# Optimization experiments

Measured on AMD Instinct MI355X. Metric: run time of the kernel, lower is better.

The kernel has to match this reference:

```python
import jax, jax.numpy as jnp
import numpy as np

B, S, IN_DIM, OUT_DIM, G = 8, 2048, 512, 256, 8
CHUNK = 128  # positions per scan step; per-chunk phi = CHUNK*O*O*G floats
EPS = 1e-5   # torch LayerNorm default


def make_periods():
    # periods[i,j,g] = i*(O*G) + j*G + g + 2
    i = jnp.arange(OUT_DIM, dtype=jnp.float32)[:, None, None]
    j = jnp.arange(OUT_DIM, dtype=jnp.float32)[None, :, None]
    g = jnp.arange(G, dtype=jnp.float32)[None, None, :]
    return i * (OUT_DIM * G) + j * G + g + 2.0


def setup_inputs() -> dict:
    key = jax.random.key(0)
    ks = jax.random.split(key, 4)
    x = jax.random.normal(ks[0], (B, S, IN_DIM), dtype=jnp.float32)
    positions = jnp.arange(S, dtype=jnp.int64 if jax.config.jax_enable_x64 else jnp.int32)
    M = jax.random.uniform(ks[1], (OUT_DIM, IN_DIM), minval=-0.5, maxval=0.5, dtype=jnp.float32)
    P = jax.random.uniform(ks[2], (OUT_DIM, OUT_DIM, G), minval=-0.1, maxval=0.1, dtype=jnp.float32)
    W_res = jax.random.uniform(ks[3], (OUT_DIM, IN_DIM), minval=-0.1, maxval=0.1, dtype=jnp.float32)
    ln_scale = jnp.ones((OUT_DIM,), dtype=jnp.float32)
    ln_bias = jnp.zeros((OUT_DIM,), dtype=jnp.float32)
    periods = make_periods()
    return {"x": x, "M": M, "P": P, "W_res": W_res, "ln_scale": ln_scale,
            "ln_bias": ln_bias, "periods": periods, "positions": positions}


def layer_norm(h, scale, bias):
    mu = jnp.mean(h, axis=-1, keepdims=True)
    var = jnp.mean(jnp.square(h - mu), axis=-1, keepdims=True)  # biased, like torch
    return (h - mu) * jax.lax.rsqrt(var + EPS) * scale + bias


def reference(x, M, P, W_res, ln_scale, ln_bias, periods, positions):
    # x: (B,S,in), M: (out,in), P: (out,out,G), periods: (out,out,G)
    x_trans = layer_norm(jnp.einsum('bsi,oi->bso', x, M), ln_scale, ln_bias)

    two_pi = jnp.float32(2.0 * np.pi)
    pos_chunks = positions.astype(jnp.float32).reshape(-1, CHUNK)  # (S/CHUNK, CHUNK)

    def body(carry, pos):
        # phi: (CHUNK, O, O, G); reduce over g first to avoid the huge 5D tensor
        phi = jnp.cos(two_pi * pos[:, None, None, None] / periods)
        A = jnp.einsum('sijg,ijg->sij', phi, P)  # (CHUNK, O, O)
        return carry, A

    _, A = jax.lax.scan(body, 0, pos_chunks)
    A = A.reshape(S, OUT_DIM, OUT_DIM)  # A[s,i,j] = sum_g P[i,j,g]*cos(2*pi*k_s/T_ijg)

    Nk = jnp.einsum('bsj,sij->bsi', x_trans, A)  # (B,S,out)
    residual = jnp.einsum('bsi,oi->bso', x, W_res)  # separate residual proj
    return Nk + residual
```

## Files before the change

### kernel.cpp

```cpp
#include <hip/hip_runtime.h>
#include <hip/hip_bf16.h>
#include <math.h>

#define B_   8
#define S_   2048
#define IN_  512
#define OUT_ 256
#define G_   8


typedef float  f32x4  __attribute__((ext_vector_type(4)));
typedef short  s16x8  __attribute__((ext_vector_type(8)));
typedef __bf16 bf16x8 __attribute__((ext_vector_type(8)));
typedef unsigned short u16x8 __attribute__((ext_vector_type(8)));

__device__ __forceinline__ float cos2pi(float f) {
#if __has_builtin(__builtin_amdgcn_cosf)
    return __builtin_amdgcn_cosf(f);
#else
    return __cosf(6.28318530717958647692f * f);
#endif
}

__device__ __forceinline__ float fractf_(float f) {
#if __has_builtin(__builtin_amdgcn_fractf)
    return __builtin_amdgcn_fractf(f);
#else
    return f - floorf(f);
#endif
}

__device__ __forceinline__ unsigned short f2bf(float f) {
    unsigned u = __builtin_bit_cast(unsigned, f);
    u += 0x7fffu + ((u >> 16) & 1u);
    return (unsigned short)(u >> 16);
}

template <typename T>
__device__ __forceinline__ auto mfma_bf16_(T a, T b, f32x4 c, int)
    -> decltype(__builtin_amdgcn_mfma_f32_16x16x32_bf16(a, b, c, 0, 0, 0)) {
    return __builtin_amdgcn_mfma_f32_16x16x32_bf16(a, b, c, 0, 0, 0);
}
template <typename T>
__device__ __forceinline__ auto mfma_bf16_(T a, T b, f32x4 c, long)
    -> decltype(__builtin_amdgcn_mfma_f32_16x16x32_bf16(__builtin_bit_cast(bf16x8, a),
                                                        __builtin_bit_cast(bf16x8, b), c, 0, 0, 0)) {
    return __builtin_amdgcn_mfma_f32_16x16x32_bf16(__builtin_bit_cast(bf16x8, a),
                                                   __builtin_bit_cast(bf16x8, b), c, 0, 0, 0);
}
__device__ __forceinline__ f32x4 mfma_bf16(s16x8 a, s16x8 b, f32x4 c) {
    return mfma_bf16_(a, b, c, 0);
}

__device__ __forceinline__ void gld16(const void* g, void* l) {
    __builtin_amdgcn_global_load_lds((const __attribute__((address_space(1))) unsigned int*)g,
                                     (__attribute__((address_space(3))) unsigned int*)l,
                                     16, 0, 0);
}

__global__ __launch_bounds__(256) void cvt_x(const float* __restrict__ x,
                                             unsigned short* __restrict__ Xb) {
    const int idx = blockIdx.x * 256 + threadIdx.x;
    const float4 v0 = *(const float4*)(x + (size_t)idx * 8);
    const float4 v1 = *(const float4*)(x + (size_t)idx * 8 + 4);
    u16x8 o;
    o[0] = f2bf(v0.x); o[1] = f2bf(v0.y); o[2] = f2bf(v0.z); o[3] = f2bf(v0.w);
    o[4] = f2bf(v1.x); o[5] = f2bf(v1.y); o[6] = f2bf(v1.z); o[7] = f2bf(v1.w);
    *(u16x8*)(Xb + (size_t)idx * 8) = o;
}

__global__ __launch_bounds__(256) void cvt_w(const float* __restrict__ M,
                                             const float* __restrict__ Wres,
                                             unsigned short* __restrict__ Wb) {
    const int idx = blockIdx.x * 256 + threadIdx.x;
    const int row = idx >> 6;
    const int col = (idx & 63) * 8;
    const float* src = (row < 256) ? (M + (size_t)row * 512 + col)
                                   : (Wres + (size_t)(row - 256) * 512 + col);
    const float4 v0 = *(const float4*)(src);
    const float4 v1 = *(const float4*)(src + 4);
    u16x8 o;
    o[0] = f2bf(v0.x); o[1] = f2bf(v0.y); o[2] = f2bf(v0.z); o[3] = f2bf(v0.w);
    o[4] = f2bf(v1.x); o[5] = f2bf(v1.y); o[6] = f2bf(v1.z); o[7] = f2bf(v1.w);
    *(u16x8*)(Wb + (size_t)row * 512 + col) = o;
}

__global__ __launch_bounds__(256) void gemm_mfma(const unsigned short* __restrict__ Xb,
                                                 const unsigned short* __restrict__ Wb,
                                                 float* __restrict__ y,
                                                 float* __restrict__ out) {
    __shared__ __align__(16) unsigned short At[128 * 64];
    __shared__ __align__(16) unsigned short Bt[128 * 64];
    const int t    = threadIdx.x;
    const int col0 = blockIdx.x * 128;
    const int row0 = blockIdx.y * 128;

    const unsigned short* ga[4];
    const unsigned short* gb[4];
    int lofs[4];
#pragma unroll
    for (int cc = 0; cc < 4; ++cc) {
        const int L = cc * 256 + t;
        const int r = L >> 3;
        const int c = (L & 7) ^ (r & 7);
        ga[cc]   = Xb + (size_t)(row0 + r) * 512 + c * 8;
        gb[cc]   = Wb + (size_t)(col0 + r) * 512 + c * 8;
        lofs[cc] = L * 8;
    }

    const int lane = t & 63;
    const int wave = t >> 6;
    const int wm   = (wave & 1) * 64;
    const int wn   = (wave >> 1) * 64;
    const int quad = lane >> 4;
    const int l16  = lane & 15;

    f32x4 acc[4][4];
#pragma unroll
    for (int mi = 0; mi < 4; ++mi)
#pragma unroll
        for (int ni = 0; ni < 4; ++ni) acc[mi][ni] = {0.0f, 0.0f, 0.0f, 0.0f};

    for (int k0 = 0; k0 < 512; k0 += 64) {
        __syncthreads();
#pragma unroll
        for (int cc = 0; cc < 4; ++cc) {
            gld16(ga[cc] + k0, At + lofs[cc]);
            gld16(gb[cc] + k0, Bt + lofs[cc]);
        }
        __syncthreads();
#pragma unroll
        for (int ks = 0; ks < 2; ++ks) {
            s16x8 af[4], bf[4];
#pragma unroll
            for (int mi = 0; mi < 4; ++mi) {
                const int cc = (ks * 4 + quad) ^ (l16 & 7);
                const int ra = wm + mi * 16 + l16;
                const int rb = wn + mi * 16 + l16;
                af[mi] = *(const s16x8*)(At + (ra * 8 + cc) * 8);
                bf[mi] = *(const s16x8*)(Bt + (rb * 8 + cc) * 8);
            }
#pragma unroll
            for (int mi = 0; mi < 4; ++mi)
#pragma unroll
                for (int ni = 0; ni < 4; ++ni)
                    acc[mi][ni] = mfma_bf16(af[mi], bf[ni], acc[mi][ni]);
        }
    }

    float* dst   = (col0 < 256) ? y : out;
    const int cb = (col0 & 255) + wn;
#pragma unroll
    for (int mi = 0; mi < 4; ++mi) {
        const int rbase = row0 + wm + mi * 16 + quad * 4;
#pragma unroll
        for (int ni = 0; ni < 4; ++ni) {
            const int col = cb + ni * 16 + l16;
#pragma unroll
            for (int rg = 0; rg < 4; ++rg)
                dst[(size_t)(rbase + rg) * 256 + col] = acc[mi][ni][rg];
        }
    }
}

__global__ __launch_bounds__(256) void gemm_kernel(const float* __restrict__ x,
                                                   const float* __restrict__ M,
                                                   const float* __restrict__ Wres,
                                                   float* __restrict__ y,
                                                   float* __restrict__ out) {
    __shared__ float As[8][132];
    __shared__ float Bs[8][132];
    const int ct = blockIdx.x;
    const int rt = blockIdx.y;
    const int t  = threadIdx.x;
    const int row0 = rt * 128;
    const float* W = (ct < 2) ? M : Wres;
    const int wcol0 = (ct & 1) * 128;
    float acc[8][8];
#pragma unroll
    for (int r = 0; r < 8; ++r)
#pragma unroll
        for (int c = 0; c < 8; ++c) acc[r][c] = 0.0f;
    const int lr = t >> 1;
    const int lk = (t & 1) << 2;
    for (int k0 = 0; k0 < 512; k0 += 8) {
        float4 av = *(const float4*)(x + (size_t)(row0 + lr) * 512 + k0 + lk);
        float4 bv = *(const float4*)(W + (size_t)(wcol0 + lr) * 512 + k0 + lk);
        __syncthreads();
        As[lk + 0][lr] = av.x; As[lk + 1][lr] = av.y; As[lk + 2][lr] = av.z; As[lk + 3][lr] = av.w;
        Bs[lk + 0][lr] = bv.x; Bs[lk + 1][lr] = bv.y; Bs[lk + 2][lr] = bv.z; Bs[lk + 3][lr] = bv.w;
        __syncthreads();
        const int tx = t & 15, ty = t >> 4;
#pragma unroll
        for (int kk = 0; kk < 8; ++kk) {
            const float4 a0 = *(const float4*)&As[kk][ty * 8];
            const float4 a1 = *(const float4*)&As[kk][ty * 8 + 4];
            const float4 b0 = *(const float4*)&Bs[kk][tx * 8];
            const float4 b1 = *(const float4*)&Bs[kk][tx * 8 + 4];
            const float ar[8] = {a0.x, a0.y, a0.z, a0.w, a1.x, a1.y, a1.z, a1.w};
            const float br[8] = {b0.x, b0.y, b0.z, b0.w, b1.x, b1.y, b1.z, b1.w};
#pragma unroll
            for (int r = 0; r < 8; ++r)
#pragma unroll
                for (int c = 0; c < 8; ++c) acc[r][c] = fmaf(ar[r], br[c], acc[r][c]);
        }
    }
    const int tx = t & 15, ty = t >> 4;
    float* dst = (ct < 2) ? y : out;
    const int cbase = (ct & 1) * 128 + tx * 8;
#pragma unroll
    for (int r = 0; r < 8; ++r) {
        float4 v0 = {acc[r][0], acc[r][1], acc[r][2], acc[r][3]};
        float4 v1 = {acc[r][4], acc[r][5], acc[r][6], acc[r][7]};
        float* p = dst + (size_t)(row0 + ty * 8 + r) * 256 + cbase;
        *(float4*)(p)     = v0;
        *(float4*)(p + 4) = v1;
    }
}

__global__ __launch_bounds__(256) void ln_kernel(float* __restrict__ y,
                                                 const float* __restrict__ scale,
                                                 const float* __restrict__ bias) {
    const int t    = threadIdx.x;
    const int row  = blockIdx.x * 4 + (t >> 6);
    const int lane = t & 63;
    float* p = y + (size_t)row * 256 + lane * 4;
    float4 v = *(float4*)p;
    float s  = v.x + v.y + v.z + v.w;
    float ss = v.x * v.x + v.y * v.y + v.z * v.z + v.w * v.w;
#pragma unroll
    for (int off = 32; off > 0; off >>= 1) {
        s  += __shfl_xor(s, off);
        ss += __shfl_xor(ss, off);
    }
    const float mu  = s * (1.0f / 256.0f);
    const float var = ss * (1.0f / 256.0f) - mu * mu;
    const float rs  = rsqrtf(var + 1e-5f);
    float4 sc = *(const float4*)(scale + lane * 4);
    float4 bi = *(const float4*)(bias + lane * 4);
    float4 o;
    o.x = (v.x - mu) * rs * sc.x + bi.x;
    o.y = (v.y - mu) * rs * sc.y + bi.y;
    o.z = (v.z - mu) * rs * sc.z + bi.z;
    o.w = (v.w - mu) * rs * sc.w + bi.w;
    *(float4*)p = o;
}

__global__ __launch_bounds__(256) void prep_ptk(const float* __restrict__ P,
                                                const float* __restrict__ periods,
                                                float4* __restrict__ PTK) {
    const int tid = blockIdx.x * 256 + threadIdx.x;
    const int j = tid >> 8, i = tid & 255;
    float p[8], iT[8], k2[8];
#pragma unroll
    for (int g = 0; g < 8; ++g) {
        const int idx = (i * 256 + j) * 8 + g;
        p[g]  = P[idx];
        iT[g] = 1.0f / periods[idx];
        k2[g] = 2.0f * cos2pi(iT[g]);
    }
    float4* base = PTK + (size_t)(j * 6) * 256 + i;
    base[0]    = make_float4(p[0], iT[0], p[1], iT[1]);
    base[256]  = make_float4(p[2], iT[2], p[3], iT[3]);
    base[512]  = make_float4(p[4], iT[4], p[5], iT[5]);
    base[768]  = make_float4(p[6], iT[6], p[7], iT[7]);
    base[1024] = make_float4(k2[0], k2[1], k2[2], k2[3]);
    base[1280] = make_float4(k2[4], k2[5], k2[6], k2[7]);
}

__global__ __launch_bounds__(256, 2) void cosnk8(const float4* __restrict__ PTK,
                                                 const float* __restrict__ xt,
                                                 float* __restrict__ out) {
    __shared__ float xs[256][64];
    const int t  = threadIdx.x;
    const int bx = blockIdx.x;
    const int ih = (bx >> 2) & 1;
    const int stile = ((bx >> 3) << 2) | (bx & 3);
    const int s0 = stile * 8;

    {
        const int slot = t >> 2;
        const int st   = slot >> 3;
        const int b    = slot & 7;
        const int jb   = (t & 3) * 64;
        const float* src = xt + (size_t)(b * S_ + s0 + st) * 256 + jb;
#pragma unroll
        for (int q = 0; q < 16; ++q) {
            float4 v = *(const float4*)(src + 4 * q);
            xs[jb + 4 * q + 0][slot] = v.x;
            xs[jb + 4 * q + 1][slot] = v.y;
            xs[jb + 4 * q + 2][slot] = v.z;
            xs[jb + 4 * q + 3][slot] = v.w;
        }
    }
    __syncthreads();

    const int i  = ih * 128 + (t & 127);
    const int jh = t >> 7;
    const int j0 = jh * 128;
    const float sv0 = (float)s0;

    float acc[8][8];
#pragma unroll
    for (int s = 0; s < 8; ++s)
#pragma unroll
        for (int b = 0; b < 8; ++b) acc[s][b] = 0.0f;

    const float4* ptk = PTK + (size_t)(j0 * 6) * 256 + i;
    float4 q0 = ptk[0],    q1 = ptk[256],  q2 = ptk[512];
    float4 q3 = ptk[768], k01 = ptk[1024], k23 = ptk[1280];

#define CHEB8(p_, iT_, k2_)                         \
    do {                                            \
        float f0 = fractf_(sv0 * (iT_));            \
        float c0 = cos2pi(f0);                      \
        float c1 = cos2pi(fractf_(f0 + (iT_)));     \
        float c2 = fmaf((k2_), c1, -c0);            \
        float c3 = fmaf((k2_), c2, -c1);            \
        float c4 = fmaf((k2_), c3, -c2);            \
        float c5 = fmaf((k2_), c4, -c3);            \
        float c6 = fmaf((k2_), c5, -c4);            \
        float c7 = fmaf((k2_), c6, -c5);            \
        a0 = fmaf((p_), c0, a0); a1 = fmaf((p_), c1, a1); \
        a2 = fmaf((p_), c2, a2); a3 = fmaf((p_), c3, a3); \
        a4 = fmaf((p_), c4, a4); a5 = fmaf((p_), c5, a5); \
        a6 = fmaf((p_), c6, a6); a7 = fmaf((p_), c7, a7); \
    } while (0)

    for (int jj = 0; jj < 128; ++jj) {
        const float4* pn = ptk + ((jj < 127) ? 1536 : 0);
        const float4 n0 = pn[0],   n1 = pn[256],  n2 = pn[512];
        const float4 n3 = pn[768], n4 = pn[1024], n5 = pn[1280];

        float a0 = 0.f, a1 = 0.f, a2 = 0.f, a3 = 0.f, a4 = 0.f, a5 = 0.f, a6 = 0.f, a7 = 0.f;
        CHEB8(q0.x, q0.y, k01.x);
        CHEB8(q0.z, q0.w, k01.y);
        CHEB8(q1.x, q1.y, k01.z);
        CHEB8(q1.z, q1.w, k01.w);
        CHEB8(q2.x, q2.y, k23.x);
        CHEB8(q2.z, q2.w, k23.y);
        CHEB8(q3.x, q3.y, k23.z);
        CHEB8(q3.z, q3.w, k23.w);

        const float* xrow = &xs[j0 + jj][0];
        const float as_[8] = {a0, a1, a2, a3, a4, a5, a6, a7};
#pragma unroll
        for (int s = 0; s < 8; ++s) {
            const float4 xa = *(const float4*)(xrow + s * 8);
            const float4 xb = *(const float4*)(xrow + s * 8 + 4);
            acc[s][0] = fmaf(as_[s], xa.x, acc[s][0]);
            acc[s][1] = fmaf(as_[s], xa.y, acc[s][1]);
            acc[s][2] = fmaf(as_[s], xa.z, acc[s][2]);
            acc[s][3] = fmaf(as_[s], xa.w, acc[s][3]);
            acc[s][4] = fmaf(as_[s], xb.x, acc[s][4]);
            acc[s][5] = fmaf(as_[s], xb.y, acc[s][5]);
            acc[s][6] = fmaf(as_[s], xb.z, acc[s][6]);
            acc[s][7] = fmaf(as_[s], xb.w, acc[s][7]);
        }
        q0 = n0; q1 = n1; q2 = n2; q3 = n3; k01 = n4; k23 = n5;
        ptk = pn;
    }
#undef CHEB8

    __syncthreads();
    float* red = &xs[0][0];
    const int tl = t & 127;
    if (jh) {
#pragma unroll
        for (int slot = 0; slot < 64; ++slot)
            red[slot * 128 + tl] = acc[slot >> 3][slot & 7];
    }
    __syncthreads();
    if (!jh) {
#pragma unroll
        for (int slot = 0; slot < 64; ++slot) {
            const int st = slot >> 3, b = slot & 7;
            const float v = acc[st][b] + red[slot * 128 + tl];
            out[(size_t)(b * S_ + s0 + st) * 256 + i] += v;
        }
    }
}

extern "C" void kernel_launch(void* const* d_in, const int* in_sizes, int n_in,
                              void* d_out, int out_size, void* d_ws, size_t ws_size,
                              hipStream_t stream) {
    const float* x        = (const float*)d_in[0];
    const float* M        = (const float*)d_in[1];
    const float* P        = (const float*)d_in[2];
    const float* Wres     = (const float*)d_in[3];
    const float* ln_scale = (const float*)d_in[4];
    const float* ln_bias  = (const float*)d_in[5];
    const float* periods  = (const float*)d_in[6];

    float* out = (float*)d_out;
    char*  wsb = (char*)d_ws;
    float* y   = (float*)wsb;
    unsigned short* Xb = (unsigned short*)(wsb + (size_t)16 * 1024 * 1024);
    float4* PTK        = (float4*)(wsb + (size_t)16 * 1024 * 1024);
    unsigned short* Wb = (unsigned short*)(wsb + (size_t)32 * 1024 * 1024);

    const bool use_mfma = (ws_size >= (size_t)34078720);

    if (use_mfma) {
        cvt_x<<<4096, 256, 0, stream>>>(x, Xb);
        cvt_w<<<128, 256, 0, stream>>>(M, Wres, Wb);
        dim3 ggrid(4, 128);
        gemm_mfma<<<ggrid, 256, 0, stream>>>(Xb, Wb, y, out);
    } else {
        dim3 ggrid(4, 128);
        gemm_kernel<<<ggrid, 256, 0, stream>>>(x, M, Wres, y, out);
    }

    ln_kernel<<<4096, 256, 0, stream>>>(y, ln_scale, ln_bias);

    prep_ptk<<<256, 256, 0, stream>>>(P, periods, PTK);

    cosnk8<<<512, 256, 0, stream>>>(PTK, y, out);
}
```

Baseline: 235.5 us.

## Split cosine kernel over j halves with atomics, shrink GEMM tile, merge conversions

The cosine/Nk kernel now splits the j reduction across two blocks, giving 1024 blocks with smaller shared memory and a higher occupancy target. Partial sums go into the output with float atomics instead of a plain read-modify-write. The MFMA GEMM moves from 128x128 to 64x128 tiles so there are twice as many blocks, and the two bf16 conversion kernels are merged into one launch. The atomics add contention and make the summation order nondeterministic, and the smaller GEMM tiles lower arithmetic intensity.

```diff
diff --git a/kernel.cpp b/kernel.cpp
--- a/kernel.cpp
+++ b/kernel.cpp
@@ -37,6 +37,16 @@
 }
 
 template <typename T>
+__device__ __forceinline__ auto atomF_(T* p, T v, int) -> decltype(unsafeAtomicAdd(p, v)) {
+    return unsafeAtomicAdd(p, v);
+}
+template <typename T>
+__device__ __forceinline__ T atomF_(T* p, T v, long) {
+    return atomicAdd(p, v);
+}
+__device__ __forceinline__ void atomAddF(float* p, float v) { atomF_(p, v, 0); }
+
+template <typename T>
 __device__ __forceinline__ auto mfma_bf16_(T a, T b, f32x4 c, int)
     -> decltype(__builtin_amdgcn_mfma_f32_16x16x32_bf16(a, b, c, 0, 0, 0)) {
     return __builtin_amdgcn_mfma_f32_16x16x32_bf16(a, b, c, 0, 0, 0);
@@ -58,92 +68,100 @@
                                      16, 0, 0);
 }
 
-__global__ __launch_bounds__(256) void cvt_x(const float* __restrict__ x,
-                                             unsigned short* __restrict__ Xb) {
-    const int idx = blockIdx.x * 256 + threadIdx.x;
-    const float4 v0 = *(const float4*)(x + (size_t)idx * 8);
-    const float4 v1 = *(const float4*)(x + (size_t)idx * 8 + 4);
-    u16x8 o;
-    o[0] = f2bf(v0.x); o[1] = f2bf(v0.y); o[2] = f2bf(v0.z); o[3] = f2bf(v0.w);
-    o[4] = f2bf(v1.x); o[5] = f2bf(v1.y); o[6] = f2bf(v1.z); o[7] = f2bf(v1.w);
-    *(u16x8*)(Xb + (size_t)idx * 8) = o;
-}
-
-__global__ __launch_bounds__(256) void cvt_w(const float* __restrict__ M,
-                                             const float* __restrict__ Wres,
-                                             unsigned short* __restrict__ Wb) {
-    const int idx = blockIdx.x * 256 + threadIdx.x;
-    const int row = idx >> 6;
-    const int col = (idx & 63) * 8;
-    const float* src = (row < 256) ? (M + (size_t)row * 512 + col)
-                                   : (Wres + (size_t)(row - 256) * 512 + col);
+__global__ __launch_bounds__(256) void cvt_xw(const float* __restrict__ x,
+                                              const float* __restrict__ M,
+                                              const float* __restrict__ Wres,
+                                              unsigned short* __restrict__ Xb,
+                                              unsigned short* __restrict__ Wb) {
+    const int bid = blockIdx.x;
+    const float* src;
+    unsigned short* dst;
+    if (bid < 4096) {
+        const int idx = bid * 256 + threadIdx.x;
+        src = x + (size_t)idx * 8;
+        dst = Xb + (size_t)idx * 8;
+    } else {
+        const int idx = (bid - 4096) * 256 + threadIdx.x;
+        const int row = idx >> 6;
+        const int col = (idx & 63) * 8;
+        src = (row < 256) ? (M + (size_t)row * 512 + col)
+                          : (Wres + (size_t)(row - 256) * 512 + col);
+        dst = Wb + (size_t)row * 512 + col;
+    }
     const float4 v0 = *(const float4*)(src);
     const float4 v1 = *(const float4*)(src + 4);
     u16x8 o;
     o[0] = f2bf(v0.x); o[1] = f2bf(v0.y); o[2] = f2bf(v0.z); o[3] = f2bf(v0.w);
     o[4] = f2bf(v1.x); o[5] = f2bf(v1.y); o[6] = f2bf(v1.z); o[7] = f2bf(v1.w);
-    *(u16x8*)(Wb + (size_t)row * 512 + col) = o;
+    *(u16x8*)dst = o;
 }
 
 __global__ __launch_bounds__(256) void gemm_mfma(const unsigned short* __restrict__ Xb,
                                                  const unsigned short* __restrict__ Wb,
                                                  float* __restrict__ y,
                                                  float* __restrict__ out) {
-    __shared__ __align__(16) unsigned short At[128 * 64];
+    __shared__ __align__(16) unsigned short At[64 * 64];
     __shared__ __align__(16) unsigned short Bt[128 * 64];
     const int t    = threadIdx.x;
     const int col0 = blockIdx.x * 128;
-    const int row0 = blockIdx.y * 128;
-
-    const unsigned short* ga[4];
-    const unsigned short* gb[4];
-    int lofs[4];
+    const int row0 = blockIdx.y * 64;
+
+    const unsigned short* ga[2]; int la[2];
+    const unsigned short* gb[4]; int lb[4];
+#pragma unroll
+    for (int cc = 0; cc < 2; ++cc) {
+        const int L = cc * 256 + t;
+        const int r = L >> 3;
+        const int c = (L & 7) ^ (r & 7);
+        ga[cc] = Xb + (size_t)(row0 + r) * 512 + c * 8;
+        la[cc] = L * 8;
+    }
 #pragma unroll
     for (int cc = 0; cc < 4; ++cc) {
         const int L = cc * 256 + t;
         const int r = L >> 3;
         const int c = (L & 7) ^ (r & 7);
-        ga[cc]   = Xb + (size_t)(row0 + r) * 512 + c * 8;
-        gb[cc]   = Wb + (size_t)(col0 + r) * 512 + c * 8;
-        lofs[cc] = L * 8;
+        gb[cc] = Wb + (size_t)(col0 + r) * 512 + c * 8;
+        lb[cc] = L * 8;
     }
 
     const int lane = t & 63;
     const int wave = t >> 6;
-    const int wm   = (wave & 1) * 64;
-    const int wn   = (wave >> 1) * 64;
+    const int wn   = wave * 32;
     const int quad = lane >> 4;
     const int l16  = lane & 15;
 
-    f32x4 acc[4][4];
+    f32x4 acc[4][2];
 #pragma unroll
     for (int mi = 0; mi < 4; ++mi)
 #pragma unroll
-        for (int ni = 0; ni < 4; ++ni) acc[mi][ni] = {0.0f, 0.0f, 0.0f, 0.0f};
+        for (int ni = 0; ni < 2; ++ni) acc[mi][ni] = {0.0f, 0.0f, 0.0f, 0.0f};
 
     for (int k0 = 0; k0 < 512; k0 += 64) {
         __syncthreads();
 #pragma unroll
-        for (int cc = 0; cc < 4; ++cc) {
-            gld16(ga[cc] + k0, At + lofs[cc]);
-            gld16(gb[cc] + k0, Bt + lofs[cc]);
-        }
+        for (int cc = 0; cc < 2; ++cc) gld16(ga[cc] + k0, At + la[cc]);
+#pragma unroll
+        for (int cc = 0; cc < 4; ++cc) gld16(gb[cc] + k0, Bt + lb[cc]);
         __syncthreads();
 #pragma unroll
         for (int ks = 0; ks < 2; ++ks) {
-            s16x8 af[4], bf[4];
+            const int cc = (ks * 4 + quad) ^ (l16 & 7);
+            s16x8 af[4], bf[2];
 #pragma unroll
             for (int mi = 0; mi < 4; ++mi) {
-                const int cc = (ks * 4 + quad) ^ (l16 & 7);
-                const int ra = wm + mi * 16 + l16;
-                const int rb = wn + mi * 16 + l16;
+                const int ra = mi * 16 + l16;
                 af[mi] = *(const s16x8*)(At + (ra * 8 + cc) * 8);
-                bf[mi] = *(const s16x8*)(Bt + (rb * 8 + cc) * 8);
             }
 #pragma unroll
+            for (int ni = 0; ni < 2; ++ni) {
+                const int rb = wn + ni * 16 + l16;
+                bf[ni] = *(const s16x8*)(Bt + (rb * 8 + cc) * 8);
+            }
+#pragma unroll
             for (int mi = 0; mi < 4; ++mi)
 #pragma unroll
-                for (int ni = 0; ni < 4; ++ni)
+                for (int ni = 0; ni < 2; ++ni)
                     acc[mi][ni] = mfma_bf16(af[mi], bf[ni], acc[mi][ni]);
         }
     }
@@ -152,9 +170,9 @@
     const int cb = (col0 & 255) + wn;
 #pragma unroll
     for (int mi = 0; mi < 4; ++mi) {
-        const int rbase = row0 + wm + mi * 16 + quad * 4;
-#pragma unroll
-        for (int ni = 0; ni < 4; ++ni) {
+        const int rbase = row0 + mi * 16 + quad * 4;
+#pragma unroll
+        for (int ni = 0; ni < 2; ++ni) {
             const int col = cb + ni * 16 + l16;
 #pragma unroll
             for (int rg = 0; rg < 4; ++rg)
@@ -268,36 +286,40 @@
     base[1280] = make_float4(k2[4], k2[5], k2[6], k2[7]);
 }
 
-__global__ __launch_bounds__(256, 2) void cosnk8(const float4* __restrict__ PTK,
-                                                 const float* __restrict__ xt,
-                                                 float* __restrict__ out) {
-    __shared__ float xs[256][64];
+__global__ __launch_bounds__(256, 4) void cosnk_js(const float4* __restrict__ PTK,
+                                                   const float* __restrict__ xt,
+                                                   float* __restrict__ out) {
+    __shared__ float xs[128 * 64];
     const int t  = threadIdx.x;
     const int bx = blockIdx.x;
     const int ih = (bx >> 2) & 1;
-    const int stile = ((bx >> 3) << 2) | (bx & 3);
+    const int rid = ((bx >> 3) << 2) | (bx & 3);
+    const int stile = rid >> 1;
+    const int jh = rid & 1;
     const int s0 = stile * 8;
+    const int jbase = jh * 128;
 
     {
         const int slot = t >> 2;
         const int st   = slot >> 3;
         const int b    = slot & 7;
-        const int jb   = (t & 3) * 64;
-        const float* src = xt + (size_t)(b * S_ + s0 + st) * 256 + jb;
-#pragma unroll
-        for (int q = 0; q < 16; ++q) {
+        const int jg   = t & 3;
+        const float* src = xt + (size_t)(b * S_ + s0 + st) * 256 + jbase + jg * 32;
+#pragma unroll
+        for (int q = 0; q < 8; ++q) {
             float4 v = *(const float4*)(src + 4 * q);
-            xs[jb + 4 * q + 0][slot] = v.x;
-            xs[jb + 4 * q + 1][slot] = v.y;
-            xs[jb + 4 * q + 2][slot] = v.z;
-            xs[jb + 4 * q + 3][slot] = v.w;
+            const int jl = jg * 32 + 4 * q;
+            xs[(jl + 0) * 64 + slot] = v.x;
+            xs[(jl + 1) * 64 + slot] = v.y;
+            xs[(jl + 2) * 64 + slot] = v.z;
+            xs[(jl + 3) * 64 + slot] = v.w;
         }
     }
     __syncthreads();
 
-    const int i  = ih * 128 + (t & 127);
-    const int jh = t >> 7;
-    const int j0 = jh * 128;
+    const int i   = ih * 128 + (t & 127);
+    const int jq  = t >> 7;
+    const int jl0 = jq * 64;
     const float sv0 = (float)s0;
 
     float acc[8][8];
@@ -306,7 +328,7 @@
 #pragma unroll
         for (int b = 0; b < 8; ++b) acc[s][b] = 0.0f;
 
-    const float4* ptk = PTK + (size_t)(j0 * 6) * 256 + i;
+    const float4* ptk = PTK + (size_t)(jbase + jl0) * 1536 + i;
     float4 q0 = ptk[0],    q1 = ptk[256],  q2 = ptk[512];
     float4 q3 = ptk[768], k01 = ptk[1024], k23 = ptk[1280];
 
@@ -327,8 +349,8 @@
         a6 = fmaf((p_), c6, a6); a7 = fmaf((p_), c7, a7); \
     } while (0)
 
-    for (int jj = 0; jj < 128; ++jj) {
-        const float4* pn = ptk + ((jj < 127) ? 1536 : 0);
+    for (int jj = 0; jj < 64; ++jj) {
+        const float4* pn = ptk + ((jj < 63) ? 1536 : 0);
         const float4 n0 = pn[0],   n1 = pn[256],  n2 = pn[512];
         const float4 n3 = pn[768], n4 = pn[1024], n5 = pn[1280];
 
@@ -342,7 +364,7 @@
         CHEB8(q3.x, q3.y, k23.z);
         CHEB8(q3.z, q3.w, k23.w);
 
-        const float* xrow = &xs[j0 + jj][0];
+        const float* xrow = &xs[(jl0 + jj) * 64];
         const float as_[8] = {a0, a1, a2, a3, a4, a5, a6, a7};
 #pragma unroll
         for (int s = 0; s < 8; ++s) {
@@ -363,20 +385,19 @@
 #undef CHEB8
 
     __syncthreads();
-    float* red = &xs[0][0];
     const int tl = t & 127;
-    if (jh) {
+    if (jq) {
 #pragma unroll
         for (int slot = 0; slot < 64; ++slot)
-            red[slot * 128 + tl] = acc[slot >> 3][slot & 7];
+            xs[slot * 128 + tl] = acc[slot >> 3][slot & 7];
     }
     __syncthreads();
-    if (!jh) {
+    if (!jq) {
 #pragma unroll
         for (int slot = 0; slot < 64; ++slot) {
             const int st = slot >> 3, b = slot & 7;
-            const float v = acc[st][b] + red[slot * 128 + tl];
-            out[(size_t)(b * S_ + s0 + st) * 256 + i] += v;
+            const float v = acc[st][b] + xs[slot * 128 + tl];
+            atomAddF(&out[(size_t)(b * S_ + s0 + st) * 256 + i], v);
         }
     }
 }
@@ -402,9 +423,8 @@
     const bool use_mfma = (ws_size >= (size_t)34078720);
 
     if (use_mfma) {
-        cvt_x<<<4096, 256, 0, stream>>>(x, Xb);
-        cvt_w<<<128, 256, 0, stream>>>(M, Wres, Wb);
-        dim3 ggrid(4, 128);
+        cvt_xw<<<4224, 256, 0, stream>>>(x, M, Wres, Xb, Wb);
+        dim3 ggrid(4, 256);
         gemm_mfma<<<ggrid, 256, 0, stream>>>(Xb, Wb, y, out);
     } else {
         dim3 ggrid(4, 128);
@@ -415,5 +435,5 @@
 
     prep_ptk<<<256, 256, 0, stream>>>(P, periods, PTK);
 
-    cosnk8<<<512, 256, 0, stream>>>(PTK, y, out);
-}
+    cosnk_js<<<1024, 256, 0, stream>>>(PTK, y, out);
+}
```

Measured after the change: 236.1 us. Within noise of the previous version (+0.3%).
